# Kernel tuning notes

Hardware: AMD Instinct MI355X
Metric: run time of the kernel (lower is better)

The kernel has to match this reference:

```python
import jax, jax.numpy as jnp
import numpy as np

NUM_EXPERTS = 8
TOP_K = 2


def setup_inputs() -> dict:
    key = jax.random.key(0)
    k1, k2 = jax.random.split(key)
    x = jax.random.normal(k1, (4, 4096, 2048), dtype=jnp.float32)
    gate_w = jax.random.normal(k2, (NUM_EXPERTS, 2048), dtype=jnp.float32) * (1.0 / np.sqrt(2048.0))
    return {"x": x, "gate_w": gate_w}


def reference(x, gate_w):
    B, T, C = x.shape
    x_flat = x.reshape(-1, C)                       # [N, C], N = B*T
    logits = jnp.einsum('nc,ec->ne', x_flat, gate_w)  # [N, E]
    probs = jax.nn.softmax(logits, axis=-1)
    weights, indices = jax.lax.top_k(probs, TOP_K)   # [N, K]
    weights = weights / jnp.sum(weights, axis=-1, keepdims=True)
    # one_hot(indices, E).sum(1): per-token multi-hot expert selection mask
    mask = jax.nn.one_hot(indices, NUM_EXPERTS, dtype=jnp.float32).sum(axis=1)  # [N, E]
    f = mask.mean(axis=0)                            # fraction of tokens per expert
    P = probs.mean(axis=0)                           # mean router prob per expert
    aux_loss = NUM_EXPERTS * jnp.sum(f * P)
    return weights, indices, aux_loss
```

## Files before the change

kernel.cpp:

```cpp
#include <hip/hip_runtime.h>

#define NTOK 16384
#define NC 2048
#define C4 512
#define NE 8
#define TPB 256
#define TOKW 2
#define TOK_PER_BLOCK 8
#define NBLK (NTOK / TOK_PER_BLOCK)

__global__ __launch_bounds__(TPB, 2) void router_kernel(
    const float* __restrict__ x, const float* __restrict__ gw,
    float* __restrict__ out, float* __restrict__ ws) {
    __shared__ float s_psum[NE];
    __shared__ float s_cnt[NE];

    const int tid = threadIdx.x;
    if (tid < NE) { s_psum[tid] = 0.0f; s_cnt[tid] = 0.0f; }
    __syncthreads();

    const int wave = tid >> 6;
    const int lane = tid & 63;
    const float4* x4 = (const float4*)x;
    const float4* gw4 = (const float4*)gw;
    const int t0 = blockIdx.x * TOK_PER_BLOCK + wave * TOKW;

    float* out_w = out;
    float* out_i = out + 2 * NTOK;

    float4 xv0[8], xv1[8];
    const float4* xr0 = x4 + (size_t)(t0 + 0) * C4 + lane;
    const float4* xr1 = x4 + (size_t)(t0 + 1) * C4 + lane;
    #pragma unroll
    for (int k = 0; k < 8; ++k) {
        xv0[k] = xr0[k * 64];
        xv1[k] = xr1[k * 64];
    }

    float acc0[NE], acc1[NE];
    #pragma unroll
    for (int e = 0; e < NE; ++e) { acc0[e] = 0.0f; acc1[e] = 0.0f; }

    #pragma unroll
    for (int k = 0; k < 8; ++k) {
        const int idx = lane + k * 64;
        #pragma unroll
        for (int e = 0; e < NE; ++e) {
            const float4 wv = gw4[e * C4 + idx];
            acc0[e] += xv0[k].x * wv.x + xv0[k].y * wv.y +
                       xv0[k].z * wv.z + xv0[k].w * wv.w;
            acc1[e] += xv1[k].x * wv.x + xv1[k].y * wv.y +
                       xv1[k].z * wv.z + xv1[k].w * wv.w;
        }
    }

    #pragma unroll
    for (int off = 32; off >= 1; off >>= 1) {
        #pragma unroll
        for (int e = 0; e < NE; ++e) {
            acc0[e] += __shfl_xor(acc0[e], off, 64);
            acc1[e] += __shfl_xor(acc1[e], off, 64);
        }
    }

    const int t = lane & 1;
    float l[NE];
    #pragma unroll
    for (int e = 0; e < NE; ++e) l[e] = t ? acc1[e] : acc0[e];

    float mx = l[0];
    #pragma unroll
    for (int e = 1; e < NE; ++e) mx = fmaxf(mx, l[e]);
    float p[NE];
    float s = 0.0f;
    #pragma unroll
    for (int e = 0; e < NE; ++e) { p[e] = expf(l[e] - mx); s += p[e]; }
    const float inv = 1.0f / s;
    #pragma unroll
    for (int e = 0; e < NE; ++e) p[e] *= inv;

    int i0 = 0; float p0 = p[0];
    #pragma unroll
    for (int e = 1; e < NE; ++e) if (p[e] > p0) { p0 = p[e]; i0 = e; }
    int i1 = (i0 == 0) ? 1 : 0; float p1 = p[i1];
    #pragma unroll
    for (int e = 0; e < NE; ++e)
        if (e != i0 && p[e] > p1) { p1 = p[e]; i1 = e; }

    if (lane < TOKW) {
        const int token = t0 + lane;
        const float wsum = p0 + p1;
        out_w[2 * token]     = p0 / wsum;
        out_w[2 * token + 1] = p1 / wsum;
        out_i[2 * token]     = (float)i0;
        out_i[2 * token + 1] = (float)i1;

        #pragma unroll
        for (int e = 0; e < NE; ++e) atomicAdd(&s_psum[e], p[e]);
        atomicAdd(&s_cnt[i0], 1.0f);
        atomicAdd(&s_cnt[i1], 1.0f);
    }

    __syncthreads();
    if (tid < NE)          ws[blockIdx.x * 16 + tid] = s_psum[tid];
    else if (tid < 2 * NE) ws[blockIdx.x * 16 + tid] = s_cnt[tid - NE];
}

__global__ void finalize_kernel(const float* __restrict__ ws,
                                float* __restrict__ out) {
    __shared__ float red[16];
    const int tid = threadIdx.x;
    if (tid < 16) red[tid] = 0.0f;
    __syncthreads();
    const int i = tid & 15;
    float sum = 0.0f;
    for (int b = (tid >> 4); b < NBLK; b += 64)
        sum += ws[b * 16 + i];
    atomicAdd(&red[i], sum);
    __syncthreads();
    if (tid == 0) {
        float aux = 0.0f;
        #pragma unroll
        for (int e = 0; e < NE; ++e)
            aux += (red[NE + e] * (1.0f / NTOK)) * (red[e] * (1.0f / NTOK));
        out[4 * NTOK] = (float)NE * aux;
    }
}

extern "C" void kernel_launch(void* const* d_in, const int* in_sizes, int n_in,
                              void* d_out, int out_size, void* d_ws, size_t ws_size,
                              hipStream_t stream) {
    const float* x  = (const float*)d_in[0];
    const float* gw = (const float*)d_in[1];
    float* out = (float*)d_out;
    float* ws  = (float*)d_ws;

    router_kernel<<<NBLK, TPB, 0, stream>>>(x, gw, out, ws);
    finalize_kernel<<<1, 1024, 0, stream>>>(ws, out);
}
```

Baseline: 52.86 us.

## Stream token rows through double-buffered LDS via global_load_lds

Each lane no longer loads its two token rows into registers up front. The kernel now copies them chunk by chunk straight into a double-buffered LDS tile using the async global-to-LDS load builtin, with a block barrier per chunk and the next chunk prefetched. The goal is lower register pressure and overlap of loads with the dot products. The cost is far fewer outstanding loads per lane and a barrier every chunk, which may reduce memory-level parallelism in this bandwidth-bound kernel.

```diff
diff --git a/kernel.cpp b/kernel.cpp
--- a/kernel.cpp
+++ b/kernel.cpp
@@ -5,52 +5,70 @@
 #define C4 512
 #define NE 8
 #define TPB 256
-#define TOKW 2
-#define TOK_PER_BLOCK 8
-#define NBLK (NTOK / TOK_PER_BLOCK)
+#define TOKB 8
+#define NBLK (NTOK / TOKB)
+#define CHUNK 64
+#define NCHUNK (C4 / CHUNK)
+
+
+typedef const unsigned int __attribute__((address_space(1)))* gk_gptr_t;
+typedef unsigned int __attribute__((address_space(3)))* gk_sptr_t;
 
 __global__ __launch_bounds__(TPB, 2) void router_kernel(
     const float* __restrict__ x, const float* __restrict__ gw,
     float* __restrict__ out, float* __restrict__ ws) {
+    __shared__ float4 tile[2][TOKB][CHUNK];
     __shared__ float s_psum[NE];
     __shared__ float s_cnt[NE];
 
     const int tid = threadIdx.x;
     if (tid < NE) { s_psum[tid] = 0.0f; s_cnt[tid] = 0.0f; }
-    __syncthreads();
 
     const int wave = tid >> 6;
     const int lane = tid & 63;
     const float4* x4 = (const float4*)x;
     const float4* gw4 = (const float4*)gw;
-    const int t0 = blockIdx.x * TOK_PER_BLOCK + wave * TOKW;
+    const int T0 = blockIdx.x * TOKB;
+    const int rA = wave;
+    const int rB = wave + 4;
+
+    const float4* srcA = x4 + (size_t)(T0 + rA) * C4 + lane;
+    const float4* srcB = x4 + (size_t)(T0 + rB) * C4 + lane;
 
     float* out_w = out;
     float* out_i = out + 2 * NTOK;
 
-    float4 xv0[8], xv1[8];
-    const float4* xr0 = x4 + (size_t)(t0 + 0) * C4 + lane;
-    const float4* xr1 = x4 + (size_t)(t0 + 1) * C4 + lane;
+    __builtin_amdgcn_global_load_lds((gk_gptr_t)(const void*)srcA,
+                                     (gk_sptr_t)(void*)&tile[0][rA][0], 16, 0, 0);
+    __builtin_amdgcn_global_load_lds((gk_gptr_t)(const void*)srcB,
+                                     (gk_sptr_t)(void*)&tile[0][rB][0], 16, 0, 0);
+
+    float accA[NE], accB[NE];
     #pragma unroll
-    for (int k = 0; k < 8; ++k) {
-        xv0[k] = xr0[k * 64];
-        xv1[k] = xr1[k * 64];
-    }
+    for (int e = 0; e < NE; ++e) { accA[e] = 0.0f; accB[e] = 0.0f; }
 
-    float acc0[NE], acc1[NE];
-    #pragma unroll
-    for (int e = 0; e < NE; ++e) { acc0[e] = 0.0f; acc1[e] = 0.0f; }
+    #pragma unroll 1
+    for (int k = 0; k < NCHUNK; ++k) {
+        const int cur = k & 1;
+        __syncthreads();
 
-    #pragma unroll
-    for (int k = 0; k < 8; ++k) {
-        const int idx = lane + k * 64;
+        if (k + 1 < NCHUNK) {
+            __builtin_amdgcn_global_load_lds(
+                (gk_gptr_t)(const void*)(srcA + (k + 1) * CHUNK),
+                (gk_sptr_t)(void*)&tile[cur ^ 1][rA][0], 16, 0, 0);
+            __builtin_amdgcn_global_load_lds(
+                (gk_gptr_t)(const void*)(srcB + (k + 1) * CHUNK),
+                (gk_sptr_t)(void*)&tile[cur ^ 1][rB][0], 16, 0, 0);
+        }
+
+        const float4 xa = tile[cur][rA][lane];
+        const float4 xb = tile[cur][rB][lane];
+        const int idx = lane + k * CHUNK;
         #pragma unroll
         for (int e = 0; e < NE; ++e) {
             const float4 wv = gw4[e * C4 + idx];
-            acc0[e] += xv0[k].x * wv.x + xv0[k].y * wv.y +
-                       xv0[k].z * wv.z + xv0[k].w * wv.w;
-            acc1[e] += xv1[k].x * wv.x + xv1[k].y * wv.y +
-                       xv1[k].z * wv.z + xv1[k].w * wv.w;
+            accA[e] += xa.x * wv.x + xa.y * wv.y + xa.z * wv.z + xa.w * wv.w;
+            accB[e] += xb.x * wv.x + xb.y * wv.y + xb.z * wv.z + xb.w * wv.w;
         }
     }
 
@@ -58,15 +76,15 @@
     for (int off = 32; off >= 1; off >>= 1) {
         #pragma unroll
         for (int e = 0; e < NE; ++e) {
-            acc0[e] += __shfl_xor(acc0[e], off, 64);
-            acc1[e] += __shfl_xor(acc1[e], off, 64);
+            accA[e] += __shfl_xor(accA[e], off, 64);
+            accB[e] += __shfl_xor(accB[e], off, 64);
         }
     }
 
     const int t = lane & 1;
     float l[NE];
     #pragma unroll
-    for (int e = 0; e < NE; ++e) l[e] = t ? acc1[e] : acc0[e];
+    for (int e = 0; e < NE; ++e) l[e] = t ? accB[e] : accA[e];
 
     float mx = l[0];
     #pragma unroll
@@ -87,8 +105,8 @@
     for (int e = 0; e < NE; ++e)
         if (e != i0 && p[e] > p1) { p1 = p[e]; i1 = e; }
 
-    if (lane < TOKW) {
-        const int token = t0 + lane;
+    if (lane < 2) {
+        const int token = T0 + (t ? rB : rA);
         const float wsum = p0 + p1;
         out_w[2 * token]     = p0 / wsum;
         out_w[2 * token + 1] = p1 / wsum;
```

New measurement: 50.73 us. -4.0%, faster.
